# Optimization experiments

Measured on AMD Instinct MI355X. Metric: run time of the kernel, lower is better.

## Reference

```python
import jax, jax.numpy as jnp
from jax import lax
import numpy as np
import math

D = 256; H = 4; DH = 64; PERIOD = 30; WIN = 4; L = 2
AUDIO = 768; MOTION = 33
B = 8; T = 1024; S = 1024


def _pe_table(t, d=D, period=PERIOD):
    pos = np.arange(period, dtype=np.float32)[:, None]
    div = np.exp(np.arange(0, d, 2, dtype=np.float32) * (-math.log(10000.0) / d))
    pe = np.zeros((period, d), np.float32)
    pe[:, 0::2] = np.sin(pos * div)
    pe[:, 1::2] = np.cos(pos * div)
    reps = t // period + 1
    return jnp.asarray(np.tile(pe, (reps, 1))[:t])


def _tgt_mask(t):
    # ALiBi-style bias (quantized by period) + causal mask, per head. [H,t,t]
    slopes = jnp.array([0.25 ** (i + 1) for i in range(H)], jnp.float32)
    i = jnp.arange(t)[:, None]
    j = jnp.arange(t)[None, :]
    rel = i - j
    alibi = jnp.where(rel >= 0, -(rel // PERIOD).astype(jnp.float32), 0.0)
    causal = jnp.where(rel >= 0, 0.0, -jnp.inf)
    return slopes[:, None, None] * alibi + causal[None]


def _mem_mask(t, s):
    i = jnp.arange(t)[:, None]
    j = jnp.arange(s)[None, :]
    return jnp.where(jnp.abs(i - j) <= WIN, 0.0, -jnp.inf)


def _ln(x, g, b, eps=1e-5):
    mu = jnp.mean(x, -1, keepdims=True)
    var = jnp.mean(jnp.square(x - mu), -1, keepdims=True)
    return (x - mu) * lax.rsqrt(var + eps) * g + b


def _mha(xq, xkv, in_w, in_b, out_w, out_b, mask):
    wq, wk, wv = jnp.split(in_w, 3, axis=0)
    bq, bk, bv = jnp.split(in_b, 3)
    q = xq @ wq.T + bq
    k = xkv @ wk.T + bk
    v = xkv @ wv.T + bv
    b_, t_, _ = q.shape
    s_ = k.shape[1]
    q = q.reshape(b_, t_, H, DH)
    k = k.reshape(b_, s_, H, DH)
    v = v.reshape(b_, s_, H, DH)
    scores = jnp.einsum('bthd,bshd->bhts', q, k) / math.sqrt(DH) + mask
    a = jax.nn.softmax(scores, axis=-1)
    o = jnp.einsum('bhts,bshd->bthd', a, v).reshape(b_, t_, D)
    return o @ out_w.T + out_b


def _conv1d(x_nch, w, b):
    y = lax.conv_general_dilated(x_nch, w, (1,), [(2, 2)],
                                 dimension_numbers=('NCH', 'OIH', 'NCH'))
    return y + b[None, :, None]


def setup_inputs() -> dict:
    key = jax.random.key(0)
    ks = iter(jax.random.split(key, 40))

    def r(shape, s=0.05):
        return jax.random.normal(next(ks), shape, jnp.float32) * s

    return {
        'hidden_states': jax.random.normal(next(ks), (B, S, AUDIO), jnp.float32),
        'target_motions': jax.random.uniform(next(ks), (B, T, MOTION), jnp.float32),
        'W_af': r((D, AUDIO)), 'b_af': r((D,)),
        'conv1_w': r((D, D, 5)), 'conv1_b': r((D,)),
        'conv2_w': r((D, D, 5)), 'conv2_b': r((D,)),
        'W_vm': r((D, MOTION)), 'b_vm': r((D,)),
        'sa_in_w': r((L, 3 * D, D)), 'sa_in_b': r((L, 3 * D)),
        'sa_out_w': r((L, D, D)), 'sa_out_b': r((L, D)),
        'ca_in_w': r((L, 3 * D, D)), 'ca_in_b': r((L, 3 * D)),
        'ca_out_w': r((L, D, D)), 'ca_out_b': r((L, D)),
        'ln1_g': jnp.ones((L, D)), 'ln1_b': jnp.zeros((L, D)),
        'ln2_g': jnp.ones((L, D)), 'ln2_b': jnp.zeros((L, D)),
        'ln3_g': jnp.ones((L, D)), 'ln3_b': jnp.zeros((L, D)),
        'ff1_w': r((L, 2 * D, D)), 'ff1_b': r((L, 2 * D)),
        'ff2_w': r((L, D, 2 * D)), 'ff2_b': r((L, D)),
        'W_vr': r((MOTION, D)), 'b_vr': r((MOTION,)),
    }


def reference(hidden_states, target_motions, W_af, b_af, conv1_w, conv1_b,
              conv2_w, conv2_b, W_vm, b_vm, sa_in_w, sa_in_b, sa_out_w,
              sa_out_b, ca_in_w, ca_in_b, ca_out_w, ca_out_b, ln1_g, ln1_b,
              ln2_g, ln2_b, ln3_g, ln3_b, ff1_w, ff1_b, ff2_w, ff2_b,
              W_vr, b_vr):
    # audio encoder: linear + residual temporal convs (exact GELU)
    audio = hidden_states @ W_af.T + b_af                       # [B,S,D]
    c = _conv1d(audio.transpose(0, 2, 1), conv1_w, conv1_b)
    c = jax.nn.gelu(c, approximate=False)
    c = _conv1d(c, conv2_w, conv2_b)
    audio = audio + c.transpose(0, 2, 1)

    b_, t_, _ = target_motions.shape
    motion_in = jnp.concatenate(
        [jnp.zeros((b_, 1, MOTION), target_motions.dtype),
         target_motions[:, :-1]], axis=1)
    x = motion_in @ W_vm.T + b_vm + _pe_table(t_)               # PPE (eval: no dropout)

    tm = _tgt_mask(t_)                                          # [H,t,t]
    mm = _mem_mask(t_, audio.shape[1])                          # [t,s]

    for l in range(L):  # post-norm TransformerDecoderLayer, relu FFN
        x = _ln(x + _mha(x, x, sa_in_w[l], sa_in_b[l], sa_out_w[l], sa_out_b[l], tm),
                ln1_g[l], ln1_b[l])
        x = _ln(x + _mha(x, audio, ca_in_w[l], ca_in_b[l], ca_out_w[l], ca_out_b[l], mm),
                ln2_g[l], ln2_b[l])
        h = jax.nn.relu(x @ ff1_w[l].T + ff1_b[l]) @ ff2_w[l].T + ff2_b[l]
        x = _ln(x + h, ln3_g[l], ln3_b[l])

    return jnp.clip(x @ W_vr.T + b_vr, 0.0, 1.0)
```

## Files before the change

### kernel.cpp

```cpp
#include <hip/hip_runtime.h>
#include <math.h>

#define B_ 8
#define T_ 1024
#define S_ 1024
#define D_ 256
#define H_ 4
#define DH_ 64
#define AUDIO_ 768
#define MOTION_ 33
#define PERIOD_ 30
#define WIN_ 4
#define M_ (B_ * T_)

typedef _Float16 half8 __attribute__((ext_vector_type(8)));
typedef _Float16 half4 __attribute__((ext_vector_type(4)));
typedef __attribute__((ext_vector_type(4))) float f32x4;

#define O_AF    0
#define O_SAIN  196608
#define O_SAOUT 589824
#define O_CAIN  720896
#define O_CAOUT 1114112
#define O_FF1   1245184
#define O_FF2   1507328
#define O_CONV1 1769472
#define O_CONV2 2097152
#define O_VR    2424832
#define WH_TOT  2441216
#define HID_TOT 6291456

struct CvtSrc { const float* p[17]; };

__global__ __launch_bounds__(256) void cvt_all(
    CvtSrc s, _Float16* __restrict__ wH, _Float16* __restrict__ hidH) {
  const long i = (long)blockIdx.x * 256 + threadIdx.x;
  if (i >= (long)WH_TOT + HID_TOT) return;
  if (i >= WH_TOT) { const long j = i - WH_TOT; hidH[j] = (_Float16)s.p[15][j]; return; }
  if (i >= O_VR) {
    const long j = i - O_VR, oc = j >> 8, cin = j & 255;
    wH[i] = (oc < MOTION_) ? (_Float16)s.p[16][oc * 256 + cin] : (_Float16)0.f;
    return;
  }
  if (i >= O_CONV2) {
    const long j = i - O_CONV2, oc = j / 1280, r = j % 1280, tap = r >> 8, cin = r & 255;
    wH[i] = (_Float16)s.p[14][(oc * 256 + cin) * 5 + tap]; return;
  }
  if (i >= O_CONV1) {
    const long j = i - O_CONV1, oc = j / 1280, r = j % 1280, tap = r >> 8, cin = r & 255;
    wH[i] = (_Float16)s.p[13][(oc * 256 + cin) * 5 + tap]; return;
  }
  int seg; long base;
  if      (i >= 1638400) { seg = 12; base = 1638400; }
  else if (i >= 1507328) { seg = 11; base = 1507328; }
  else if (i >= 1376256) { seg = 10; base = 1376256; }
  else if (i >= 1245184) { seg = 9;  base = 1245184; }
  else if (i >= 1179648) { seg = 8;  base = 1179648; }
  else if (i >= 1114112) { seg = 7;  base = 1114112; }
  else if (i >= 917504)  { seg = 6;  base = 917504; }
  else if (i >= 720896)  { seg = 5;  base = 720896; }
  else if (i >= 655360)  { seg = 4;  base = 655360; }
  else if (i >= 589824)  { seg = 3;  base = 589824; }
  else if (i >= 393216)  { seg = 2;  base = 393216; }
  else if (i >= 196608)  { seg = 1;  base = 196608; }
  else                   { seg = 0;  base = 0; }
  wH[i] = (_Float16)s.p[seg][i - base];
}

__global__ __launch_bounds__(256) void gemm_h(
    const _Float16* __restrict__ A, const _Float16* __restrict__ W,
    const float* __restrict__ bias, float* __restrict__ Cf,
    _Float16* __restrict__ Ch, int M, int N, int K, int relu) {
  __shared__ _Float16 As[2][64][72];
  __shared__ _Float16 Bs[2][64][72];
  const int tid = threadIdx.x;
  const int wave = tid >> 6, lane = tid & 63;
  const int wr = wave >> 1, wc = wave & 1;
  const int lr16 = lane & 15, kq = lane >> 4;
  const int bm = blockIdx.x, bn = blockIdx.y;
  const int sr = tid >> 2, sq = tid & 3;

  const _Float16* Ap = A + (size_t)(bm * 64 + sr) * K + sq * 8;
  const _Float16* Wp = W + (size_t)(bn * 64 + sr) * K + sq * 8;

  half8 ra0 = *reinterpret_cast<const half8*>(Ap);
  half8 ra1 = *reinterpret_cast<const half8*>(Ap + 32);
  half8 rw0 = *reinterpret_cast<const half8*>(Wp);
  half8 rw1 = *reinterpret_cast<const half8*>(Wp + 32);
  f32x4 acc[2][2] = {};

  *reinterpret_cast<half8*>(&As[0][sr][sq * 8]) = ra0;
  *reinterpret_cast<half8*>(&As[0][sr][32 + sq * 8]) = ra1;
  *reinterpret_cast<half8*>(&Bs[0][sr][sq * 8]) = rw0;
  *reinterpret_cast<half8*>(&Bs[0][sr][32 + sq * 8]) = rw1;
  __syncthreads();

  const int nsteps = K >> 6;
  for (int step = 0; step < nsteps; ++step) {
    const int cur = step & 1;
    const bool more = (step + 1 < nsteps);
    if (more) {
      const int kn = (step + 1) << 6;
      ra0 = *reinterpret_cast<const half8*>(Ap + kn);
      ra1 = *reinterpret_cast<const half8*>(Ap + kn + 32);
      rw0 = *reinterpret_cast<const half8*>(Wp + kn);
      rw1 = *reinterpret_cast<const half8*>(Wp + kn + 32);
    }
    half8 af[2][2], bf[2][2];
#pragma unroll
    for (int m = 0; m < 2; ++m)
#pragma unroll
      for (int s = 0; s < 2; ++s)
        af[m][s] = *reinterpret_cast<const half8*>(
            &As[cur][wr * 32 + m * 16 + lr16][s * 32 + kq * 8]);
#pragma unroll
    for (int n = 0; n < 2; ++n)
#pragma unroll
      for (int s = 0; s < 2; ++s)
        bf[n][s] = *reinterpret_cast<const half8*>(
            &Bs[cur][wc * 32 + n * 16 + lr16][s * 32 + kq * 8]);
#pragma unroll
    for (int m = 0; m < 2; ++m)
#pragma unroll
      for (int n = 0; n < 2; ++n)
#pragma unroll
        for (int s = 0; s < 2; ++s)
          acc[m][n] = __builtin_amdgcn_mfma_f32_16x16x32_f16(af[m][s], bf[n][s], acc[m][n], 0, 0, 0);
    if (more) {
      *reinterpret_cast<half8*>(&As[cur ^ 1][sr][sq * 8]) = ra0;
      *reinterpret_cast<half8*>(&As[cur ^ 1][sr][32 + sq * 8]) = ra1;
      *reinterpret_cast<half8*>(&Bs[cur ^ 1][sr][sq * 8]) = rw0;
      *reinterpret_cast<half8*>(&Bs[cur ^ 1][sr][32 + sq * 8]) = rw1;
      __syncthreads();
    }
  }

#pragma unroll
  for (int m = 0; m < 2; ++m) {
#pragma unroll
    for (int n = 0; n < 2; ++n) {
      const int col = bn * 64 + wc * 32 + n * 16 + lr16;
      const float bv = bias[col];
#pragma unroll
      for (int j = 0; j < 4; ++j) {
        const int row = bm * 64 + wr * 32 + m * 16 + kq * 4 + j;
        float v = acc[m][n][j] + bv;
        if (relu) v = fmaxf(v, 0.f);
        const size_t idx = (size_t)row * N + col;
        if (Cf) Cf[idx] = v;
        if (Ch) Ch[idx] = (_Float16)v;
      }
    }
  }
}

__device__ __forceinline__ half8 conv_ld(const _Float16* Xb, int p, int tap, int cin) {
  const int sp = p + tap - 2;
  if (sp < 0 || sp >= S_) { half8 z = {}; return z; }
  return *reinterpret_cast<const half8*>(Xb + (size_t)sp * D_ + cin);
}

__global__ __launch_bounds__(256) void conv_h(
    const _Float16* __restrict__ Xh, const _Float16* __restrict__ Wc,
    const float* __restrict__ bias, _Float16* __restrict__ OutH,
    const float* __restrict__ ResF, int mode) {
  __shared__ _Float16 As[2][64][72];
  __shared__ _Float16 Bs[2][64][72];
  const int tid = threadIdx.x;
  const int wave = tid >> 6, lane = tid & 63;
  const int wr = wave >> 1, wc = wave & 1;
  const int lr16 = lane & 15, kq = lane >> 4;
  const int b = blockIdx.x >> 4;
  const int s0 = (blockIdx.x & 15) * 64;
  const int o0 = blockIdx.y * 64;
  const int sr = tid >> 2, sq = tid & 3;

  const _Float16* Xb = Xh + (size_t)b * S_ * D_;
  const _Float16* Wp = Wc + (size_t)(o0 + sr) * 1280 + sq * 8;
  const int p = s0 + sr;

  half8 ra0 = conv_ld(Xb, p, 0, sq * 8);
  half8 ra1 = conv_ld(Xb, p, 0, 32 + sq * 8);
  half8 rw0 = *reinterpret_cast<const half8*>(Wp);
  half8 rw1 = *reinterpret_cast<const half8*>(Wp + 32);
  f32x4 acc[2][2] = {};

  *reinterpret_cast<half8*>(&As[0][sr][sq * 8]) = ra0;
  *reinterpret_cast<half8*>(&As[0][sr][32 + sq * 8]) = ra1;
  *reinterpret_cast<half8*>(&Bs[0][sr][sq * 8]) = rw0;
  *reinterpret_cast<half8*>(&Bs[0][sr][32 + sq * 8]) = rw1;
  __syncthreads();

  for (int step = 0; step < 20; ++step) {
    const int cur = step & 1;
    const bool more = (step + 1 < 20);
    if (more) {
      const int kn = (step + 1) << 6;
      const int tap = kn >> 8, cb = kn & 255;
      ra0 = conv_ld(Xb, p, tap, cb + sq * 8);
      ra1 = conv_ld(Xb, p, tap, cb + 32 + sq * 8);
      rw0 = *reinterpret_cast<const half8*>(Wp + kn);
      rw1 = *reinterpret_cast<const half8*>(Wp + kn + 32);
    }
    half8 af[2][2], bf[2][2];
#pragma unroll
    for (int m = 0; m < 2; ++m)
#pragma unroll
      for (int s = 0; s < 2; ++s)
        af[m][s] = *reinterpret_cast<const half8*>(
            &As[cur][wr * 32 + m * 16 + lr16][s * 32 + kq * 8]);
#pragma unroll
    for (int n = 0; n < 2; ++n)
#pragma unroll
      for (int s = 0; s < 2; ++s)
        bf[n][s] = *reinterpret_cast<const half8*>(
            &Bs[cur][wc * 32 + n * 16 + lr16][s * 32 + kq * 8]);
#pragma unroll
    for (int m = 0; m < 2; ++m)
#pragma unroll
      for (int n = 0; n < 2; ++n)
#pragma unroll
        for (int s = 0; s < 2; ++s)
          acc[m][n] = __builtin_amdgcn_mfma_f32_16x16x32_f16(af[m][s], bf[n][s], acc[m][n], 0, 0, 0);
    if (more) {
      *reinterpret_cast<half8*>(&As[cur ^ 1][sr][sq * 8]) = ra0;
      *reinterpret_cast<half8*>(&As[cur ^ 1][sr][32 + sq * 8]) = ra1;
      *reinterpret_cast<half8*>(&Bs[cur ^ 1][sr][sq * 8]) = rw0;
      *reinterpret_cast<half8*>(&Bs[cur ^ 1][sr][32 + sq * 8]) = rw1;
      __syncthreads();
    }
  }

#pragma unroll
  for (int m = 0; m < 2; ++m) {
#pragma unroll
    for (int n = 0; n < 2; ++n) {
      const int oc = o0 + wc * 32 + n * 16 + lr16;
      const float bv = bias[oc];
#pragma unroll
      for (int j = 0; j < 4; ++j) {
        const int s = s0 + wr * 32 + m * 16 + kq * 4 + j;
        const size_t idx = ((size_t)b * S_ + s) * D_ + oc;
        float v = acc[m][n][j] + bv;
        if (mode == 0) {
          v = 0.5f * v * (1.f + erff(v * 0.70710678118654752f));
        } else {
          v += ResF[idx];
        }
        OutH[idx] = (_Float16)v;
      }
    }
  }
}

__global__ __launch_bounds__(256) void head_mfma(
    const _Float16* __restrict__ Xh, const _Float16* __restrict__ Wh,
    const float* __restrict__ bv, float* __restrict__ Out) {
  __shared__ _Float16 As[2][64][72];
  __shared__ _Float16 Bs[2][64][72];
  const int tid = threadIdx.x;
  const int wave = tid >> 6, lane = tid & 63;
  const int wr = wave >> 1, wc = wave & 1;
  const int lr16 = lane & 15, kq = lane >> 4;
  const int bm = blockIdx.x;
  const int sr = tid >> 2, sq = tid & 3;

  const _Float16* Ap = Xh + (size_t)(bm * 64 + sr) * D_ + sq * 8;
  const _Float16* Wp = Wh + (size_t)sr * D_ + sq * 8;

  half8 ra0 = *reinterpret_cast<const half8*>(Ap);
  half8 ra1 = *reinterpret_cast<const half8*>(Ap + 32);
  half8 rw0 = *reinterpret_cast<const half8*>(Wp);
  half8 rw1 = *reinterpret_cast<const half8*>(Wp + 32);
  f32x4 acc[2][2] = {};

  *reinterpret_cast<half8*>(&As[0][sr][sq * 8]) = ra0;
  *reinterpret_cast<half8*>(&As[0][sr][32 + sq * 8]) = ra1;
  *reinterpret_cast<half8*>(&Bs[0][sr][sq * 8]) = rw0;
  *reinterpret_cast<half8*>(&Bs[0][sr][32 + sq * 8]) = rw1;
  __syncthreads();

  for (int step = 0; step < 4; ++step) {
    const int cur = step & 1;
    const bool more = (step + 1 < 4);
    if (more) {
      const int kn = (step + 1) << 6;
      ra0 = *reinterpret_cast<const half8*>(Ap + kn);
      ra1 = *reinterpret_cast<const half8*>(Ap + kn + 32);
      rw0 = *reinterpret_cast<const half8*>(Wp + kn);
      rw1 = *reinterpret_cast<const half8*>(Wp + kn + 32);
    }
    half8 af[2][2], bf[2][2];
#pragma unroll
    for (int m = 0; m < 2; ++m)
#pragma unroll
      for (int s = 0; s < 2; ++s)
        af[m][s] = *reinterpret_cast<const half8*>(
            &As[cur][wr * 32 + m * 16 + lr16][s * 32 + kq * 8]);
#pragma unroll
    for (int n = 0; n < 2; ++n)
#pragma unroll
      for (int s = 0; s < 2; ++s)
        bf[n][s] = *reinterpret_cast<const half8*>(
            &Bs[cur][wc * 32 + n * 16 + lr16][s * 32 + kq * 8]);
#pragma unroll
    for (int m = 0; m < 2; ++m)
#pragma unroll
      for (int n = 0; n < 2; ++n)
#pragma unroll
        for (int s = 0; s < 2; ++s)
          acc[m][n] = __builtin_amdgcn_mfma_f32_16x16x32_f16(af[m][s], bf[n][s], acc[m][n], 0, 0, 0);
    if (more) {
      *reinterpret_cast<half8*>(&As[cur ^ 1][sr][sq * 8]) = ra0;
      *reinterpret_cast<half8*>(&As[cur ^ 1][sr][32 + sq * 8]) = ra1;
      *reinterpret_cast<half8*>(&Bs[cur ^ 1][sr][sq * 8]) = rw0;
      *reinterpret_cast<half8*>(&Bs[cur ^ 1][sr][32 + sq * 8]) = rw1;
      __syncthreads();
    }
  }

#pragma unroll
  for (int m = 0; m < 2; ++m) {
#pragma unroll
    for (int n = 0; n < 2; ++n) {
      const int col = wc * 32 + n * 16 + lr16;
      if (col < MOTION_) {
        const float bb = bv[col];
#pragma unroll
        for (int j = 0; j < 4; ++j) {
          const int row = bm * 64 + wr * 32 + m * 16 + kq * 4 + j;
          float v = acc[m][n][j] + bb;
          Out[(size_t)row * MOTION_ + col] = fminf(fmaxf(v, 0.f), 1.f);
        }
      }
    }
  }
}

__global__ __launch_bounds__(256) void motion_pe(
    const float* __restrict__ TM, const float* __restrict__ Wvm,
    const float* __restrict__ bvm, float* __restrict__ Xout,
    _Float16* __restrict__ XoutH) {
  const int d = threadIdx.x;
  const int bt = blockIdx.x;
  const int t = bt & (T_ - 1);
  const int b = bt >> 10;
  float acc = bvm[d];
  if (t > 0) {
    const float* mrow = TM + ((size_t)b * T_ + t - 1) * MOTION_;
    const float* wrow = Wvm + (size_t)d * MOTION_;
#pragma unroll
    for (int m = 0; m < MOTION_; ++m) acc += mrow[m] * wrow[m];
  }
  const int pos = t % PERIOD_;
  const int i2 = d >> 1;
  const float div = expf((float)(2 * i2) * (-9.210340371976184f / 256.f));
  const float ang = (float)pos * div;
  acc += (d & 1) ? cosf(ang) : sinf(ang);
  Xout[(size_t)bt * D_ + d] = acc;
  XoutH[(size_t)bt * D_ + d] = (_Float16)acc;
}

#define RSK_ 72
#define RSV_ 64
__global__ __launch_bounds__(512) void self_attn(
    const _Float16* __restrict__ QKV, _Float16* __restrict__ O) {
  __shared__ _Float16 Ks[2][64 * RSK_];
  __shared__ _Float16 VTs[2][64 * RSV_];
  __shared__ _Float16 Ps[8][16 * RSK_];
  const int qtb = blockIdx.x, h = blockIdx.y, b = blockIdx.z;
  const int tid = threadIdx.x;
  const int wave = tid >> 6, lane = tid & 63;
  const int lo = lane & 15, hi = lane >> 4;
  const float slope = exp2f(-2.f * (float)(h + 1));
  const int qloc = wave * 16 + lo;
  const int tq = qtb * 128 + qloc;
  const size_t base = (size_t)b * T_ * 768 + h * 64;
  const int sj = tid >> 3, sch = tid & 7;

  half8 qf[2];
#pragma unroll
  for (int s = 0; s < 2; ++s)
    qf[s] = *reinterpret_cast<const half8*>(
        QKV + base + (size_t)(qtb * 128 + qloc) * 768 + s * 32 + hi * 8);

  f32x4 oacc[4] = {};
  float mrun = -1e30f, lrun = 0.f;

  const int nkt = 2 * qtb + 2;

  half8 rk, rv;
  {
    const size_t rowoff = base + (size_t)sj * 768;
    rk = *reinterpret_cast<const half8*>(QKV + rowoff + 256 + sch * 8);
    rv = *reinterpret_cast<const half8*>(QKV + rowoff + 512 + sch * 8);
    *reinterpret_cast<half8*>(&Ks[0][sj * RSK_ + sch * 8]) = rk;
#pragma unroll
    for (int r = 0; r < 8; ++r) {
      const int d = sch * 8 + r;
      const int sw = ((d & 7) ^ (d >> 3)) << 3;
      VTs[0][d * RSV_ + (sj ^ sw)] = rv[r];
    }
  }
  __syncthreads();

  for (int kt = 0; kt < nkt; ++kt) {
    const int cur = kt & 1;
    const bool more = (kt + 1 < nkt);
    if (more) {
      const size_t rowoff = base + (size_t)((kt + 1) * 64 + sj) * 768;
      rk = *reinterpret_cast<const half8*>(QKV + rowoff + 256 + sch * 8);
      rv = *reinterpret_cast<const half8*>(QKV + rowoff + 512 + sch * 8);
    }

    f32x4 st[4] = {};
#pragma unroll
    for (int f = 0; f < 4; ++f) {
#pragma unroll
      for (int s = 0; s < 2; ++s) {
        const half8 kf = *reinterpret_cast<const half8*>(
            &Ks[cur][(f * 16 + lo) * RSK_ + s * 32 + hi * 8]);
        st[f] = __builtin_amdgcn_mfma_f32_16x16x32_f16(kf, qf[s], st[f], 0, 0, 0);
      }
    }

    float sc[4][4];
    float tmax = -1e30f;
#pragma unroll
    for (int f = 0; f < 4; ++f)
#pragma unroll
      for (int r = 0; r < 4; ++r) {
        const int j = kt * 64 + f * 16 + hi * 4 + r;
        const int rel = tq - j;
        const float v = (rel >= 0)
            ? st[f][r] * 0.125f - slope * (float)(rel / PERIOD_) : -1e30f;
        sc[f][r] = v;
        tmax = fmaxf(tmax, v);
      }
    tmax = fmaxf(tmax, __shfl_xor(tmax, 16, 64));
    tmax = fmaxf(tmax, __shfl_xor(tmax, 32, 64));
    const float mnew = fmaxf(mrun, tmax);
    const float scale = __expf(mrun - mnew);

    float psum = 0.f;
#pragma unroll
    for (int f = 0; f < 4; ++f) {
      half4 ph;
#pragma unroll
      for (int r = 0; r < 4; ++r) {
        const float pv = __expf(sc[f][r] - mnew);
        psum += pv;
        ph[r] = (_Float16)pv;
      }
      *reinterpret_cast<half4*>(&Ps[wave][lo * RSK_ + f * 16 + hi * 4]) = ph;
    }
    psum += __shfl_xor(psum, 16, 64);
    psum += __shfl_xor(psum, 32, 64);
    lrun = lrun * scale + psum;
    mrun = mnew;

    float rsc[4];
#pragma unroll
    for (int r = 0; r < 4; ++r) rsc[r] = __shfl(scale, hi * 4 + r, 64);
#pragma unroll
    for (int nf = 0; nf < 4; ++nf)
#pragma unroll
      for (int r = 0; r < 4; ++r) oacc[nf][r] *= rsc[r];

#pragma unroll
    for (int s = 0; s < 2; ++s) {
      const half8 pf = *reinterpret_cast<const half8*>(
          &Ps[wave][lo * RSK_ + s * 32 + hi * 8]);
#pragma unroll
      for (int nf = 0; nf < 4; ++nf) {
        const int d = nf * 16 + lo;
        const int sw = ((d & 7) ^ (d >> 3)) << 3;
        const half8 vf = *reinterpret_cast<const half8*>(
            &VTs[cur][d * RSV_ + ((s * 32 + hi * 8) ^ sw)]);
        oacc[nf] = __builtin_amdgcn_mfma_f32_16x16x32_f16(pf, vf, oacc[nf], 0, 0, 0);
      }
    }

    if (more) {
      *reinterpret_cast<half8*>(&Ks[cur ^ 1][sj * RSK_ + sch * 8]) = rk;
#pragma unroll
      for (int r = 0; r < 8; ++r) {
        const int d = sch * 8 + r;
        const int sw = ((d & 7) ^ (d >> 3)) << 3;
        VTs[cur ^ 1][d * RSV_ + (sj ^ sw)] = rv[r];
      }
      __syncthreads();
    }
  }

  float invl[4];
#pragma unroll
  for (int r = 0; r < 4; ++r) invl[r] = 1.f / __shfl(lrun, hi * 4 + r, 64);
#pragma unroll
  for (int nf = 0; nf < 4; ++nf)
#pragma unroll
    for (int r = 0; r < 4; ++r) {
      const int q = qtb * 128 + wave * 16 + hi * 4 + r;
      O[((size_t)b * T_ + q) * D_ + h * 64 + nf * 16 + lo] =
          (_Float16)(oacc[nf][r] * invl[r]);
    }
}

__global__ __launch_bounds__(256) void cross_attn(
    const _Float16* __restrict__ Q, const _Float16* __restrict__ KV,
    _Float16* __restrict__ O) {
  const int gid = blockIdx.x * 256 + threadIdx.x;
  const int h = gid & 3;
  const int bt = gid >> 2;
  const int t = bt & (T_ - 1);
  const int b = bt >> 10;

  float q[64];
  const _Float16* qp = Q + (size_t)bt * D_ + h * 64;
#pragma unroll
  for (int d0 = 0; d0 < 64; d0 += 8) {
    const half8 v = *reinterpret_cast<const half8*>(qp + d0);
#pragma unroll
    for (int e = 0; e < 8; ++e) q[d0 + e] = (float)v[e];
  }

  const int j0 = (t - WIN_ > 0) ? t - WIN_ : 0;
  const int j1 = (t + WIN_ < S_ - 1) ? t + WIN_ : S_ - 1;
  const int nj = j1 - j0 + 1;

  float sc[9];
  float mx = -1e30f;
#pragma unroll
  for (int jj = 0; jj < 9; ++jj) {
    if (jj < nj) {
      const _Float16* kp = KV + ((size_t)b * S_ + j0 + jj) * 512 + h * 64;
      float s = 0.f;
#pragma unroll
      for (int d0 = 0; d0 < 64; d0 += 8) {
        const half8 kv = *reinterpret_cast<const half8*>(kp + d0);
#pragma unroll
        for (int e = 0; e < 8; ++e) s += q[d0 + e] * (float)kv[e];
      }
      sc[jj] = s * 0.125f;
      mx = fmaxf(mx, sc[jj]);
    } else {
      sc[jj] = -1e30f;
    }
  }
  float l = 0.f;
  float p[9];
#pragma unroll
  for (int jj = 0; jj < 9; ++jj) { p[jj] = __expf(sc[jj] - mx); l += p[jj]; }
  const float inv = 1.f / l;

  float o[64];
#pragma unroll
  for (int d = 0; d < 64; ++d) o[d] = 0.f;
#pragma unroll
  for (int jj = 0; jj < 9; ++jj) {
    if (jj < nj) {
      const float pj = p[jj] * inv;
      const _Float16* vp = KV + ((size_t)b * S_ + j0 + jj) * 512 + 256 + h * 64;
#pragma unroll
      for (int d0 = 0; d0 < 64; d0 += 8) {
        const half8 vv = *reinterpret_cast<const half8*>(vp + d0);
#pragma unroll
        for (int e = 0; e < 8; ++e) o[d0 + e] += pj * (float)vv[e];
      }
    }
  }
  _Float16* op = O + (size_t)bt * D_ + h * 64;
#pragma unroll
  for (int d = 0; d < 64; ++d) op[d] = (_Float16)o[d];
}

__global__ __launch_bounds__(256) void ln_res(
    const float* X, const float* __restrict__ R,
    const float* __restrict__ g, const float* __restrict__ bta,
    float* Out, _Float16* __restrict__ OutH) {
  const int wid = threadIdx.x >> 6, lane = threadIdx.x & 63;
  const size_t row = (size_t)blockIdx.x * 4 + wid;
  const float* xp = X + row * D_;
  const float* rp = R + row * D_;
  float v[4];
  float s = 0.f;
#pragma unroll
  for (int k = 0; k < 4; ++k) {
    const int d = lane + k * 64;
    v[k] = xp[d] + rp[d];
    s += v[k];
  }
#pragma unroll
  for (int off = 32; off; off >>= 1) s += __shfl_xor(s, off, 64);
  const float mu = s * (1.f / 256.f);
  float var = 0.f;
#pragma unroll
  for (int k = 0; k < 4; ++k) { const float d = v[k] - mu; var += d * d; }
#pragma unroll
  for (int off = 32; off; off >>= 1) var += __shfl_xor(var, off, 64);
  const float rs = rsqrtf(var * (1.f / 256.f) + 1e-5f);
#pragma unroll
  for (int k = 0; k < 4; ++k) {
    const int d = lane + k * 64;
    const float o = (v[k] - mu) * rs * g[d] + bta[d];
    Out[row * D_ + d] = o;
    OutH[row * D_ + d] = (_Float16)o;
  }
}

extern "C" void kernel_launch(void* const* d_in, const int* in_sizes, int n_in,
                              void* d_out, int out_size, void* d_ws, size_t ws_size,
                              hipStream_t stream) {
  (void)in_sizes; (void)n_in; (void)out_size; (void)ws_size;
  const float* hidden = (const float*)d_in[0];
  const float* tmot   = (const float*)d_in[1];
  const float* W_af   = (const float*)d_in[2];
  const float* b_af   = (const float*)d_in[3];
  const float* c1w    = (const float*)d_in[4];
  const float* c1b    = (const float*)d_in[5];
  const float* c2w    = (const float*)d_in[6];
  const float* c2b    = (const float*)d_in[7];
  const float* Wvm    = (const float*)d_in[8];
  const float* bvm    = (const float*)d_in[9];
  const float* sa_in_w  = (const float*)d_in[10];
  const float* sa_in_b  = (const float*)d_in[11];
  const float* sa_out_w = (const float*)d_in[12];
  const float* sa_out_b = (const float*)d_in[13];
  const float* ca_in_w  = (const float*)d_in[14];
  const float* ca_in_b  = (const float*)d_in[15];
  const float* ca_out_w = (const float*)d_in[16];
  const float* ca_out_b = (const float*)d_in[17];
  const float* ln1g = (const float*)d_in[18];
  const float* ln1b = (const float*)d_in[19];
  const float* ln2g = (const float*)d_in[20];
  const float* ln2b = (const float*)d_in[21];
  const float* ln3g = (const float*)d_in[22];
  const float* ln3b = (const float*)d_in[23];
  const float* ff1w = (const float*)d_in[24];
  const float* ff1b = (const float*)d_in[25];
  const float* ff2w = (const float*)d_in[26];
  const float* ff2b = (const float*)d_in[27];
  const float* Wvr  = (const float*)d_in[28];
  const float* bvr  = (const float*)d_in[29];
  float* out = (float*)d_out;

  float* ws = (float*)d_ws;
  const size_t BSD = (size_t)M_ * D_;
  float* audio = ws;
  float* x     = ws + BSD;
  float* t1    = ws + 2 * BSD;
  _Float16* hb = (_Float16*)(ws + 3 * BSD);
  _Float16* Rh      = hb;
  _Float16* x_h     = hb + 3 * BSD;
  _Float16* audio_h = hb + 4 * BSD;
  _Float16* att_h   = hb + 5 * BSD;
  _Float16* wH      = hb + 6 * BSD;
  _Float16* ckv_h   = Rh + BSD;

  const dim3 blk(256);

  CvtSrc cs;
  cs.p[0] = W_af;
  cs.p[1] = sa_in_w;            cs.p[2] = sa_in_w + 768 * 256;
  cs.p[3] = sa_out_w;           cs.p[4] = sa_out_w + 256 * 256;
  cs.p[5] = ca_in_w;            cs.p[6] = ca_in_w + 768 * 256;
  cs.p[7] = ca_out_w;           cs.p[8] = ca_out_w + 256 * 256;
  cs.p[9] = ff1w;               cs.p[10] = ff1w + 512 * 256;
  cs.p[11] = ff2w;              cs.p[12] = ff2w + 256 * 512;
  cs.p[13] = c1w;               cs.p[14] = c2w;
  cs.p[15] = hidden;            cs.p[16] = Wvr;
  cvt_all<<<dim3((WH_TOT + HID_TOT + 255) / 256), blk, 0, stream>>>(cs, wH, Rh);

  gemm_h<<<dim3(M_ / 64, 4), blk, 0, stream>>>(Rh, wH + O_AF, b_af, audio, audio_h,
                                               M_, 256, 768, 0);
  conv_h<<<dim3(128, 4), blk, 0, stream>>>(audio_h, wH + O_CONV1, c1b, Rh, nullptr, 0);
  conv_h<<<dim3(128, 4), blk, 0, stream>>>(Rh, wH + O_CONV2, c2b, audio_h, audio, 1);

  motion_pe<<<dim3(M_), blk, 0, stream>>>(tmot, Wvm, bvm, x, x_h);

  for (int l = 0; l < 2; ++l) {
    gemm_h<<<dim3(M_ / 64, 12), blk, 0, stream>>>(
        x_h, wH + O_SAIN + l * 196608, sa_in_b + l * 768, nullptr, Rh, M_, 768, 256, 0);
    self_attn<<<dim3(T_ / 128, H_, B_), dim3(512), 0, stream>>>(Rh, att_h);
    gemm_h<<<dim3(M_ / 64, 4), blk, 0, stream>>>(
        att_h, wH + O_SAOUT + l * 65536, sa_out_b + l * 256, t1, nullptr, M_, 256, 256, 0);
    ln_res<<<dim3(M_ / 4), blk, 0, stream>>>(x, t1, ln1g + l * 256, ln1b + l * 256, x, x_h);

    gemm_h<<<dim3(M_ / 64, 4), blk, 0, stream>>>(
        x_h, wH + O_CAIN + l * 196608, ca_in_b + l * 768, nullptr, Rh, M_, 256, 256, 0);
    gemm_h<<<dim3(M_ / 64, 8), blk, 0, stream>>>(
        audio_h, wH + O_CAIN + l * 196608 + 65536, ca_in_b + l * 768 + 256,
        nullptr, ckv_h, M_, 512, 256, 0);
    cross_attn<<<dim3(M_ * H_ / 256), blk, 0, stream>>>(Rh, ckv_h, att_h);
    gemm_h<<<dim3(M_ / 64, 4), blk, 0, stream>>>(
        att_h, wH + O_CAOUT + l * 65536, ca_out_b + l * 256, t1, nullptr, M_, 256, 256, 0);
    ln_res<<<dim3(M_ / 4), blk, 0, stream>>>(x, t1, ln2g + l * 256, ln2b + l * 256, x, x_h);

    gemm_h<<<dim3(M_ / 64, 8), blk, 0, stream>>>(
        x_h, wH + O_FF1 + l * 131072, ff1b + l * 512, nullptr, Rh, M_, 512, 256, 1);
    gemm_h<<<dim3(M_ / 64, 4), blk, 0, stream>>>(
        Rh, wH + O_FF2 + l * 131072, ff2b + l * 256, t1, nullptr, M_, 256, 512, 0);
    ln_res<<<dim3(M_ / 4), blk, 0, stream>>>(x, t1, ln3g + l * 256, ln3b + l * 256, x, x_h);
  }

  head_mfma<<<dim3(M_ / 64), blk, 0, stream>>>(x_h, wH + O_VR, bvr, out);
}
```

Measured before the change: 363.4 us.

## Store GEMM outputs in fp16, merge cross-attn Q/KV projections, shrink cross_attn blocks

The sublayer output GEMMs now write fp16 into a half buffer, and ln_res reads it instead of fp32, roughly halving that intermediate traffic. The fp32 audio copy is dropped and the conv residual reads the fp16 audio in place. The cross-attention Q and KV projections are merged into one gemm_ca launch, and cross_attn uses 128-thread blocks for more blocks. Residual and sublayer values now pass through fp16, so precision drops a little, and the in-place conv aliasing relies on each element being read and written by the same thread.

```diff
diff --git a/kernel.cpp b/kernel.cpp
--- a/kernel.cpp
+++ b/kernel.cpp
@@ -154,6 +154,93 @@
   }
 }
 
+__global__ __launch_bounds__(256) void gemm_ca(
+    const _Float16* __restrict__ Aq, const _Float16* __restrict__ Akv,
+    const _Float16* __restrict__ W, const float* __restrict__ bias,
+    _Float16* __restrict__ Oq, _Float16* __restrict__ Okv) {
+  __shared__ _Float16 As[2][64][72];
+  __shared__ _Float16 Bs[2][64][72];
+  const int tid = threadIdx.x;
+  const int wave = tid >> 6, lane = tid & 63;
+  const int wr = wave >> 1, wc = wave & 1;
+  const int lr16 = lane & 15, kq = lane >> 4;
+  const int bm = blockIdx.x, bn = blockIdx.y;
+  const int sr = tid >> 2, sq = tid & 3;
+  const bool isq = (bn < 4);
+  const _Float16* A = isq ? Aq : Akv;
+  _Float16* Optr = isq ? Oq : Okv;
+  const int Nout = isq ? 256 : 512;
+  const int ocol0 = (isq ? bn : bn - 4) * 64;
+
+  const _Float16* Ap = A + (size_t)(bm * 64 + sr) * 256 + sq * 8;
+  const _Float16* Wp = W + (size_t)(bn * 64 + sr) * 256 + sq * 8;
+
+  half8 ra0 = *reinterpret_cast<const half8*>(Ap);
+  half8 ra1 = *reinterpret_cast<const half8*>(Ap + 32);
+  half8 rw0 = *reinterpret_cast<const half8*>(Wp);
+  half8 rw1 = *reinterpret_cast<const half8*>(Wp + 32);
+  f32x4 acc[2][2] = {};
+
+  *reinterpret_cast<half8*>(&As[0][sr][sq * 8]) = ra0;
+  *reinterpret_cast<half8*>(&As[0][sr][32 + sq * 8]) = ra1;
+  *reinterpret_cast<half8*>(&Bs[0][sr][sq * 8]) = rw0;
+  *reinterpret_cast<half8*>(&Bs[0][sr][32 + sq * 8]) = rw1;
+  __syncthreads();
+
+  for (int step = 0; step < 4; ++step) {
+    const int cur = step & 1;
+    const bool more = (step + 1 < 4);
+    if (more) {
+      const int kn = (step + 1) << 6;
+      ra0 = *reinterpret_cast<const half8*>(Ap + kn);
+      ra1 = *reinterpret_cast<const half8*>(Ap + kn + 32);
+      rw0 = *reinterpret_cast<const half8*>(Wp + kn);
+      rw1 = *reinterpret_cast<const half8*>(Wp + kn + 32);
+    }
+    half8 af[2][2], bf[2][2];
+#pragma unroll
+    for (int m = 0; m < 2; ++m)
+#pragma unroll
+      for (int s = 0; s < 2; ++s)
+        af[m][s] = *reinterpret_cast<const half8*>(
+            &As[cur][wr * 32 + m * 16 + lr16][s * 32 + kq * 8]);
+#pragma unroll
+    for (int n = 0; n < 2; ++n)
+#pragma unroll
+      for (int s = 0; s < 2; ++s)
+        bf[n][s] = *reinterpret_cast<const half8*>(
+            &Bs[cur][wc * 32 + n * 16 + lr16][s * 32 + kq * 8]);
+#pragma unroll
+    for (int m = 0; m < 2; ++m)
+#pragma unroll
+      for (int n = 0; n < 2; ++n)
+#pragma unroll
+        for (int s = 0; s < 2; ++s)
+          acc[m][n] = __builtin_amdgcn_mfma_f32_16x16x32_f16(af[m][s], bf[n][s], acc[m][n], 0, 0, 0);
+    if (more) {
+      *reinterpret_cast<half8*>(&As[cur ^ 1][sr][sq * 8]) = ra0;
+      *reinterpret_cast<half8*>(&As[cur ^ 1][sr][32 + sq * 8]) = ra1;
+      *reinterpret_cast<half8*>(&Bs[cur ^ 1][sr][sq * 8]) = rw0;
+      *reinterpret_cast<half8*>(&Bs[cur ^ 1][sr][32 + sq * 8]) = rw1;
+      __syncthreads();
+    }
+  }
+
+#pragma unroll
+  for (int m = 0; m < 2; ++m) {
+#pragma unroll
+    for (int n = 0; n < 2; ++n) {
+      const int lc = wc * 32 + n * 16 + lr16;
+      const float bv = bias[bn * 64 + lc];
+#pragma unroll
+      for (int j = 0; j < 4; ++j) {
+        const int row = bm * 64 + wr * 32 + m * 16 + kq * 4 + j;
+        Optr[(size_t)row * Nout + ocol0 + lc] = (_Float16)(acc[m][n][j] + bv);
+      }
+    }
+  }
+}
+
 __device__ __forceinline__ half8 conv_ld(const _Float16* Xb, int p, int tap, int cin) {
   const int sp = p + tap - 2;
   if (sp < 0 || sp >= S_) { half8 z = {}; return z; }
@@ -162,8 +249,8 @@
 
 __global__ __launch_bounds__(256) void conv_h(
     const _Float16* __restrict__ Xh, const _Float16* __restrict__ Wc,
-    const float* __restrict__ bias, _Float16* __restrict__ OutH,
-    const float* __restrict__ ResF, int mode) {
+    const float* __restrict__ bias, _Float16* OutH,
+    const _Float16* ResH, int mode) {
   __shared__ _Float16 As[2][64][72];
   __shared__ _Float16 Bs[2][64][72];
   const int tid = threadIdx.x;
@@ -245,7 +332,7 @@
         if (mode == 0) {
           v = 0.5f * v * (1.f + erff(v * 0.70710678118654752f));
         } else {
-          v += ResF[idx];
+          v += (float)ResH[idx];
         }
         OutH[idx] = (_Float16)v;
       }
@@ -506,10 +593,10 @@
     }
 }
 
-__global__ __launch_bounds__(256) void cross_attn(
+__global__ __launch_bounds__(128) void cross_attn(
     const _Float16* __restrict__ Q, const _Float16* __restrict__ KV,
     _Float16* __restrict__ O) {
-  const int gid = blockIdx.x * 256 + threadIdx.x;
+  const int gid = blockIdx.x * 128 + threadIdx.x;
   const int h = gid & 3;
   const int bt = gid >> 2;
   const int t = bt & (T_ - 1);
@@ -575,19 +662,19 @@
 }
 
 __global__ __launch_bounds__(256) void ln_res(
-    const float* X, const float* __restrict__ R,
+    const float* X, const _Float16* __restrict__ R,
     const float* __restrict__ g, const float* __restrict__ bta,
     float* Out, _Float16* __restrict__ OutH) {
   const int wid = threadIdx.x >> 6, lane = threadIdx.x & 63;
   const size_t row = (size_t)blockIdx.x * 4 + wid;
   const float* xp = X + row * D_;
-  const float* rp = R + row * D_;
+  const _Float16* rp = R + row * D_;
   float v[4];
   float s = 0.f;
 #pragma unroll
   for (int k = 0; k < 4; ++k) {
     const int d = lane + k * 64;
-    v[k] = xp[d] + rp[d];
+    v[k] = xp[d] + (float)rp[d];
     s += v[k];
   }
 #pragma unroll
@@ -646,9 +733,8 @@
 
   float* ws = (float*)d_ws;
   const size_t BSD = (size_t)M_ * D_;
-  float* audio = ws;
   float* x     = ws + BSD;
-  float* t1    = ws + 2 * BSD;
+  _Float16* t1h = (_Float16*)(ws + 2 * BSD);
   _Float16* hb = (_Float16*)(ws + 3 * BSD);
   _Float16* Rh      = hb;
   _Float16* x_h     = hb + 3 * BSD;
@@ -671,10 +757,10 @@
   cs.p[15] = hidden;            cs.p[16] = Wvr;
   cvt_all<<<dim3((WH_TOT + HID_TOT + 255) / 256), blk, 0, stream>>>(cs, wH, Rh);
 
-  gemm_h<<<dim3(M_ / 64, 4), blk, 0, stream>>>(Rh, wH + O_AF, b_af, audio, audio_h,
+  gemm_h<<<dim3(M_ / 64, 4), blk, 0, stream>>>(Rh, wH + O_AF, b_af, nullptr, audio_h,
                                                M_, 256, 768, 0);
-  conv_h<<<dim3(128, 4), blk, 0, stream>>>(audio_h, wH + O_CONV1, c1b, Rh, nullptr, 0);
-  conv_h<<<dim3(128, 4), blk, 0, stream>>>(Rh, wH + O_CONV2, c2b, audio_h, audio, 1);
+  conv_h<<<dim3(128, 4), blk, 0, stream>>>(audio_h, wH + O_CONV1, c1b, t1h, nullptr, 0);
+  conv_h<<<dim3(128, 4), blk, 0, stream>>>(t1h, wH + O_CONV2, c2b, audio_h, audio_h, 1);
 
   motion_pe<<<dim3(M_), blk, 0, stream>>>(tmot, Wvm, bvm, x, x_h);
 
@@ -683,24 +769,21 @@
         x_h, wH + O_SAIN + l * 196608, sa_in_b + l * 768, nullptr, Rh, M_, 768, 256, 0);
     self_attn<<<dim3(T_ / 128, H_, B_), dim3(512), 0, stream>>>(Rh, att_h);
     gemm_h<<<dim3(M_ / 64, 4), blk, 0, stream>>>(
-        att_h, wH + O_SAOUT + l * 65536, sa_out_b + l * 256, t1, nullptr, M_, 256, 256, 0);
-    ln_res<<<dim3(M_ / 4), blk, 0, stream>>>(x, t1, ln1g + l * 256, ln1b + l * 256, x, x_h);
-
+        att_h, wH + O_SAOUT + l * 65536, sa_out_b + l * 256, nullptr, t1h, M_, 256, 256, 0);
+    ln_res<<<dim3(M_ / 4), blk, 0, stream>>>(x, t1h, ln1g + l * 256, ln1b + l * 256, x, x_h);
+
+    gemm_ca<<<dim3(M_ / 64, 12), blk, 0, stream>>>(
+        x_h, audio_h, wH + O_CAIN + l * 196608, ca_in_b + l * 768, Rh, ckv_h);
+    cross_attn<<<dim3(M_ * H_ / 128), dim3(128), 0, stream>>>(Rh, ckv_h, att_h);
     gemm_h<<<dim3(M_ / 64, 4), blk, 0, stream>>>(
-        x_h, wH + O_CAIN + l * 196608, ca_in_b + l * 768, nullptr, Rh, M_, 256, 256, 0);
-    gemm_h<<<dim3(M_ / 64, 8), blk, 0, stream>>>(
-        audio_h, wH + O_CAIN + l * 196608 + 65536, ca_in_b + l * 768 + 256,
-        nullptr, ckv_h, M_, 512, 256, 0);
-    cross_attn<<<dim3(M_ * H_ / 256), blk, 0, stream>>>(Rh, ckv_h, att_h);
-    gemm_h<<<dim3(M_ / 64, 4), blk, 0, stream>>>(
-        att_h, wH + O_CAOUT + l * 65536, ca_out_b + l * 256, t1, nullptr, M_, 256, 256, 0);
-    ln_res<<<dim3(M_ / 4), blk, 0, stream>>>(x, t1, ln2g + l * 256, ln2b + l * 256, x, x_h);
+        att_h, wH + O_CAOUT + l * 65536, ca_out_b + l * 256, nullptr, t1h, M_, 256, 256, 0);
+    ln_res<<<dim3(M_ / 4), blk, 0, stream>>>(x, t1h, ln2g + l * 256, ln2b + l * 256, x, x_h);
 
     gemm_h<<<dim3(M_ / 64, 8), blk, 0, stream>>>(
         x_h, wH + O_FF1 + l * 131072, ff1b + l * 512, nullptr, Rh, M_, 512, 256, 1);
     gemm_h<<<dim3(M_ / 64, 4), blk, 0, stream>>>(
-        Rh, wH + O_FF2 + l * 131072, ff2b + l * 256, t1, nullptr, M_, 256, 512, 0);
-    ln_res<<<dim3(M_ / 4), blk, 0, stream>>>(x, t1, ln3g + l * 256, ln3b + l * 256, x, x_h);
+        Rh, wH + O_FF2 + l * 131072, ff2b + l * 256, nullptr, t1h, M_, 256, 512, 0);
+    ln_res<<<dim3(M_ / 4), blk, 0, stream>>>(x, t1h, ln3g + l * 256, ln3b + l * 256, x, x_h);
   }
 
   head_mfma<<<dim3(M_ / 64), blk, 0, stream>>>(x_h, wH + O_VR, bvr, out);
```

Measured after the change: 334.9 us. -7.8%, faster.
